# Kernel optimization log

Hardware: AMD Instinct MI355X
Metric: run time of the kernel (lower is better)

## Reference

```python
import jax, jax.numpy as jnp
import numpy as np

B, L, D = 2, 1024, 768
NH, HD = 12, 64
NL = 6
MLP = 3072
THETA = 10000.0


def _rope(pos, dim, theta):
    # pos: (L,) float -> (L, dim//2, 2, 2) rotation matrices (FLUX rope)
    omega = 1.0 / (theta ** (jnp.arange(0, dim, 2, dtype=jnp.float32) / dim))
    out = pos[:, None] * omega  # (L, dim//2)
    cos, sin = jnp.cos(out), jnp.sin(out)
    return jnp.stack([jnp.stack([cos, -sin], -1), jnp.stack([sin, cos], -1)], -2)


def _build_pe(seq_len, pe_dim):
    # 2D spatial ids: axis0 = x (fast), axis1 = y (slow); axes_dim = [pe_dim//2, pe_dim//2]
    h = w = int(seq_len ** 0.5)
    y_ids = jnp.repeat(jnp.arange(h, dtype=jnp.float32), w)
    x_ids = jnp.tile(jnp.arange(w, dtype=jnp.float32), h)
    half = pe_dim // 2
    pe = jnp.concatenate([_rope(x_ids, half, THETA), _rope(y_ids, half, THETA)], axis=-3)
    return pe[None, None]  # (1, 1, L, pe_dim//2, 2, 2)


def _apply_rope(x, pe):
    # x: (B, H, L, HD)
    xs = x.reshape(x.shape[:-1] + (-1, 1, 2))
    out = pe[..., 0] * xs[..., 0] + pe[..., 1] * xs[..., 1]
    return out.reshape(x.shape)


def _rmsnorm(x, scale):
    return x * jax.lax.rsqrt(jnp.mean(x * x, axis=-1, keepdims=True) + 1e-6) * scale


def _layernorm(x, g, b):
    m = jnp.mean(x, axis=-1, keepdims=True)
    v = jnp.var(x, axis=-1, keepdims=True)
    return (x - m) * jax.lax.rsqrt(v + 1e-5) * g + b


def _forward(spatial_features, density_weights, condition_embeddings,
             spatial_w, spatial_b, cond_w, cond_b,
             ln1_g, ln1_b, qkv_w, q_scale, k_scale, proj_w, proj_b,
             dscale, dbias, ln2_g, ln2_b, mlp_w1, mlp_b1, mlp_w2, mlp_b2,
             out_w, out_b):
    Bsz, Ls, Ds = spatial_features.shape
    x = spatial_features @ spatial_w + spatial_b
    x = x + (condition_embeddings @ cond_w + cond_b)[:, None, :]
    pe = _build_pe(Ls, HD)
    dflat = density_weights.reshape(Bsz, 1, Ls)  # H*W == L, no interpolation
    attn_scale = HD ** -0.5
    for i in range(NL):
        h = _layernorm(x, ln1_g[i], ln1_b[i])
        qkv = (h @ qkv_w[i]).reshape(Bsz, Ls, 3, NH, HD).transpose(2, 0, 3, 1, 4)
        q, k, v = qkv[0], qkv[1], qkv[2]
        q = _rmsnorm(q, q_scale[i])
        k = _rmsnorm(k, k_scale[i])
        q = _apply_rope(q, pe)
        k = _apply_rope(k, pe)
        scores = jnp.einsum('bhld,bhmd->bhlm', q, k) * attn_scale
        scores = scores + (dscale[i] * dflat[..., None] + dbias[i])  # (B,1,L,1) bcast
        attn = jax.nn.softmax(scores, axis=-1)
        o = jnp.einsum('bhlm,bhmd->bhld', attn, v)
        o = o.transpose(0, 2, 1, 3).reshape(Bsz, Ls, Ds)
        x = x + o @ proj_w[i] + proj_b[i]
        h2 = _layernorm(x, ln2_g[i], ln2_b[i])
        x = x + jax.nn.gelu(h2 @ mlp_w1[i] + mlp_b1[i], approximate=False) @ mlp_w2[i] + mlp_b2[i]
    return x @ out_w + out_b


def setup_inputs() -> dict:
    key = jax.random.key(0)
    ks = jax.random.split(key, 16)
    s = 0.02
    inp = {
        'spatial_features': jax.random.normal(ks[0], (B, L, D), jnp.float32),
        'density_weights': jax.random.uniform(ks[1], (B, 32, 32), jnp.float32),
        'condition_embeddings': jax.random.normal(ks[2], (B, 1536), jnp.float32),
        'spatial_w': jax.random.normal(ks[3], (D, D), jnp.float32) * s,
        'spatial_b': jnp.zeros((D,), jnp.float32),
        'cond_w': jax.random.normal(ks[4], (1536, D), jnp.float32) * s,
        'cond_b': jnp.zeros((D,), jnp.float32),
        'ln1_g': jnp.ones((NL, D), jnp.float32),
        'ln1_b': jnp.zeros((NL, D), jnp.float32),
        'qkv_w': jax.random.normal(ks[5], (NL, D, 3 * D), jnp.float32) * s,
        'q_scale': jnp.ones((NL, HD), jnp.float32),
        'k_scale': jnp.ones((NL, HD), jnp.float32),
        'proj_w': jax.random.normal(ks[6], (NL, D, D), jnp.float32) * s,
        'proj_b': jnp.zeros((NL, D), jnp.float32),
        'dscale': jnp.ones((NL,), jnp.float32),
        'dbias': jnp.zeros((NL,), jnp.float32),
        'ln2_g': jnp.ones((NL, D), jnp.float32),
        'ln2_b': jnp.zeros((NL, D), jnp.float32),
        'mlp_w1': jax.random.normal(ks[7], (NL, D, MLP), jnp.float32) * s,
        'mlp_b1': jnp.zeros((NL, MLP), jnp.float32),
        'mlp_w2': jax.random.normal(ks[8], (NL, MLP, D), jnp.float32) * s,
        'mlp_b2': jnp.zeros((NL, D), jnp.float32),
        'out_w': jax.random.normal(ks[9], (D, D), jnp.float32) * s,
        'out_b': jnp.zeros((D,), jnp.float32),
    }
    return inp


def reference(spatial_features, density_weights, condition_embeddings,
              spatial_w, spatial_b, cond_w, cond_b,
              ln1_g, ln1_b, qkv_w, q_scale, k_scale, proj_w, proj_b,
              dscale, dbias, ln2_g, ln2_b, mlp_w1, mlp_b1, mlp_w2, mlp_b2,
              out_w, out_b):
    return _forward(spatial_features, density_weights, condition_embeddings,
                    spatial_w, spatial_b, cond_w, cond_b,
                    ln1_g, ln1_b, qkv_w, q_scale, k_scale, proj_w, proj_b,
                    dscale, dbias, ln2_g, ln2_b, mlp_w1, mlp_b1, mlp_w2, mlp_b2,
                    out_w, out_b)
```

## Files before the change

### kernel.cpp

```cpp
#include <hip/hip_runtime.h>
#include <hip/hip_bf16.h>
#include <cstdint>
#include <cstddef>

typedef unsigned short u16;
using short8  = __attribute__((ext_vector_type(8))) short;
using floatx4 = __attribute__((ext_vector_type(4))) float;

typedef __attribute__((address_space(1))) void gvoid;
typedef __attribute__((address_space(3))) void svoid;

__device__ __forceinline__ u16 f2bf(float f) {
  __hip_bfloat16 h = __float2bfloat16(f);
  return __builtin_bit_cast(u16, h);
}

__device__ __forceinline__ floatx4 mfma16(short8 a, short8 b, floatx4 c) {
  return __builtin_amdgcn_mfma_f32_16x16x32_bf16(a, b, c, 0, 0, 0);
}

__device__ __forceinline__ void glds16(const u16* g, u16* l) {
  __builtin_amdgcn_global_load_lds((gvoid*)g, (svoid*)l, 16, 0, 0);
}

__global__ void pe_kernel(float* __restrict__ pet) {
  int t = blockIdx.x * 256 + threadIdx.x;
  if (t >= 32768) return;
  int l = t >> 5, j = t & 31;
  float pos   = (j < 16) ? (float)(l & 31) : (float)(l >> 5);
  float omega = powf(10000.f, -(float)(j & 15) / 16.f);
  float a = pos * omega;
  pet[2 * t]     = cosf(a);
  pet[2 * t + 1] = sinf(a);
}

__global__ __launch_bounds__(256) void twt_kernel(const float* __restrict__ in,
                                                  u16* __restrict__ out, int K, int N) {
  size_t lofs = (size_t)blockIdx.z * K * N;
  in  += lofs;
  out += lofs;
  __shared__ float tile[32][33];
  int bx = blockIdx.x;
  int by = blockIdx.y;
  int t = threadIdx.x;
  int lk = t >> 3, ln = (t & 7) * 4;
  float4 v = *(const float4*)(in + (size_t)(by * 32 + lk) * N + bx * 32 + ln);
  tile[lk][ln + 0] = v.x; tile[lk][ln + 1] = v.y;
  tile[lk][ln + 2] = v.z; tile[lk][ln + 3] = v.w;
  __syncthreads();
  int n = t >> 3, k0 = (t & 7) * 4;
  ushort4 o;
  o.x = f2bf(tile[k0 + 0][n]); o.y = f2bf(tile[k0 + 1][n]);
  o.z = f2bf(tile[k0 + 2][n]); o.w = f2bf(tile[k0 + 3][n]);
  *(ushort4*)(out + (size_t)(bx * 32 + n) * K + by * 32 + k0) = o;
}

__global__ void cvt_kernel(const float* __restrict__ in, u16* __restrict__ out, int n) {
  int i = blockIdx.x * 256 + threadIdx.x;
  if (i < n) out[i] = f2bf(in[i]);
}

__global__ __launch_bounds__(256) void condp_kernel(const float* __restrict__ ce,
                                                    const float* __restrict__ w,
                                                    float* __restrict__ partial) {
  int d = blockIdx.x * 256 + threadIdx.x;
  int c = blockIdx.y;
  #pragma unroll
  for (int b = 0; b < 2; b++) {
    float acc = 0.f;
    #pragma unroll 4
    for (int k = c * 96; k < c * 96 + 96; k++) acc += ce[b * 1536 + k] * w[(size_t)k * 768 + d];
    partial[(size_t)(c * 2 + b) * 768 + d] = acc;
  }
}

__global__ __launch_bounds__(256) void condr_kernel(const float* __restrict__ partial,
                                                    const float* __restrict__ bias,
                                                    float* __restrict__ out) {
  int t = blockIdx.x * 256 + threadIdx.x;
  int b = t / 768, d = t % 768;
  float acc = bias[d];
  #pragma unroll
  for (int c = 0; c < 16; c++) acc += partial[(size_t)(c * 2 + b) * 768 + d];
  out[b * 768 + d] = acc;
}

__global__ __launch_bounds__(256) void ln_kernel(const float* __restrict__ x,
                                                 const float* __restrict__ g,
                                                 const float* __restrict__ b,
                                                 u16* __restrict__ out) {
  int row = blockIdx.x;
  const float* xr = x + (size_t)row * 768;
  int t = threadIdx.x;
  float v0 = xr[t], v1 = xr[t + 256], v2 = xr[t + 512];
  float s = v0 + v1 + v2, s2 = v0 * v0 + v1 * v1 + v2 * v2;
  #pragma unroll
  for (int o = 32; o >= 1; o >>= 1) { s += __shfl_xor(s, o); s2 += __shfl_xor(s2, o); }
  __shared__ float red[8];
  int w = t >> 6, lane = t & 63;
  if (lane == 0) { red[w] = s; red[4 + w] = s2; }
  __syncthreads();
  s  = red[0] + red[1] + red[2] + red[3];
  s2 = red[4] + red[5] + red[6] + red[7];
  float mean = s * (1.f / 768.f);
  float var  = s2 * (1.f / 768.f) - mean * mean;
  float rstd = rsqrtf(var + 1e-5f);
  u16* orow = out + (size_t)row * 768;
  orow[t]       = f2bf((v0 - mean) * rstd * g[t] + b[t]);
  orow[t + 256] = f2bf((v1 - mean) * rstd * g[t + 256] + b[t + 256]);
  orow[t + 512] = f2bf((v2 - mean) * rstd * g[t + 512] + b[t + 512]);
}

__global__ __launch_bounds__(256) void vtransb_kernel(const u16* __restrict__ vb,
                                                      u16* __restrict__ vt) {
  int lt = blockIdx.x, bh = blockIdx.y;
  int b = bh / 12, h = bh % 12;
  __shared__ u16 tile[64][72];
  int t = threadIdx.x;
  int lr = t >> 2, c0 = (t & 3) * 16;
  const u16* src = vb + (size_t)(b * 1024 + lt * 64 + lr) * 768 + h * 64 + c0;
  *(short8*)&tile[lr][c0]     = *(const short8*)src;
  *(short8*)&tile[lr][c0 + 8] = *(const short8*)(src + 8);
  __syncthreads();
  int d = t >> 2, l0 = (t & 3) * 16;
  u16 o[16];
  #pragma unroll
  for (int i = 0; i < 16; i++) o[i] = tile[l0 + i][d];
  u16* dst = vt + ((size_t)bh * 64 + d) * 1024 + lt * 64 + l0;
  *(short8*)dst       = *(short8*)&o[0];
  *(short8*)(dst + 8) = *(short8*)&o[8];
}

__global__ __launch_bounds__(256) void attn_split(const u16* __restrict__ qb,
                                                  const u16* __restrict__ kbuf,
                                                  const u16* __restrict__ vt,
                                                  float* __restrict__ po,
                                                  float* __restrict__ pl) {
  const int qt = blockIdx.x, bh = blockIdx.y, sp = blockIdx.z;
  const int lane = threadIdx.x & 63, w = threadIdx.x >> 6;
  const int quad = lane >> 4, l16 = lane & 15;
  __shared__ __align__(16) u16 Ks[128 * 64];
  __shared__ __align__(16) u16 Vs[64 * 128];
  __shared__ __align__(16) u16 Ps[4][16 * 136];
  const u16* Q  = qb   + (size_t)bh * 1024 * 64;
  const u16* Kp = kbuf + (size_t)bh * 1024 * 64;
  const u16* Vp = vt   + (size_t)bh * 64 * 1024;
  const int qrow0 = qt * 64 + w * 16;
  short8 aq0, aq1;
  {
    const u16* qp = Q + (size_t)(qrow0 + l16) * 64 + quad * 8;
    aq0 = *(const short8*)qp;
    aq1 = *(const short8*)(qp + 32);
  }
  floatx4 accO[4];
  #pragma unroll
  for (int i = 0; i < 4; i++) accO[i] = (floatx4){0.f, 0.f, 0.f, 0.f};
  float lsum[4] = {0.f, 0.f, 0.f, 0.f};

  const int krow_in = (lane >> 3);
  const int kchunk  = lane & 7;
  const int vrow_in = (lane >> 4);
  const int vchunk  = lane & 15;

  for (int nt = 0; nt < 4; ++nt) {
    const int kb0 = sp * 512 + nt * 128;
    __syncthreads();
    #pragma unroll
    for (int j = 0; j < 4; j++) {
      int r = w * 32 + j * 8 + krow_in;
      int g = kchunk ^ (r & 7);
      glds16(Kp + (size_t)(kb0 + r) * 64 + g * 8, Ks + (w * 32 + j * 8) * 64);
    }
    #pragma unroll
    for (int j = 0; j < 4; j++) {
      int r = w * 16 + j * 4 + vrow_in;
      int g = vchunk ^ (r & 15);
      glds16(Vp + (size_t)r * 1024 + kb0 + g * 8, Vs + (w * 16 + j * 4) * 128);
    }
    __syncthreads();

    floatx4 s[8];
    #pragma unroll
    for (int n = 0; n < 8; n++) {
      int row = n * 16 + l16;
      int c0 = quad ^ (l16 & 7);
      short8 b0 = *(const short8*)&Ks[row * 64 + c0 * 8];
      short8 b1 = *(const short8*)&Ks[row * 64 + (c0 ^ 4) * 8];
      floatx4 z = (floatx4){0.f, 0.f, 0.f, 0.f};
      z = mfma16(aq0, b0, z);
      s[n] = mfma16(aq1, b1, z);
    }
    #pragma unroll
    for (int n = 0; n < 8; n++) {
      #pragma unroll
      for (int r = 0; r < 4; r++) {
        float pv = __expf(s[n][r] - 8.f);
        lsum[r] += pv;
        Ps[w][(quad * 4 + r) * 136 + n * 16 + l16] = f2bf(pv);
      }
    }
    #pragma unroll
    for (int kt = 0; kt < 4; kt++) {
      short8 ap = *(const short8*)&Ps[w][l16 * 136 + kt * 32 + quad * 8];
      #pragma unroll
      for (int dt = 0; dt < 4; dt++) {
        int vrow = dt * 16 + l16;
        int c = (kt * 4 + quad) ^ l16;
        short8 bv = *(const short8*)&Vs[vrow * 128 + c * 8];
        accO[dt] = mfma16(ap, bv, accO[dt]);
      }
    }
  }
  #pragma unroll
  for (int r = 0; r < 4; r++) {
    #pragma unroll
    for (int o = 1; o < 16; o <<= 1) lsum[r] += __shfl_xor(lsum[r], o);
  }
  const size_t sb = (size_t)(sp * 24 + bh) * 1024;
  #pragma unroll
  for (int r = 0; r < 4; r++) {
    int lr = qrow0 + quad * 4 + r;
    if (l16 == 0) pl[sb + lr] = lsum[r];
    #pragma unroll
    for (int dt = 0; dt < 4; dt++)
      po[(sb + lr) * 64 + dt * 16 + l16] = accO[dt][r];
  }
}

__global__ __launch_bounds__(256) void attn_comb(const float* __restrict__ po,
                                                 const float* __restrict__ pl,
                                                 u16* __restrict__ obuf) {
  int w = threadIdx.x >> 6, lane = threadIdx.x & 63;
  int gr = blockIdx.x * 4 + w;
  int bh = gr >> 10, l = gr & 1023;
  float num = 0.f, den = 0.f;
  #pragma unroll
  for (int s = 0; s < 2; s++) {
    num += po[((size_t)(s * 24 + bh) * 1024 + l) * 64 + lane];
    den += pl[(size_t)(s * 24 + bh) * 1024 + l];
  }
  int b = bh / 12, h = bh % 12;
  obuf[((size_t)(b * 1024 + l)) * 768 + h * 64 + lane] = f2bf(num / den);
}

template <int EPI, int BM, int BN>
__global__ __launch_bounds__(256) void gemm_bt(const u16* __restrict__ A,
                                               const u16* __restrict__ Bt,
                                               const float* __restrict__ bias,
                                               const float* extra,
                                               float* Cf, u16* Cb, int M, int N, int K,
                                               const float* qsc, const float* ksc,
                                               const float* petp,
                                               u16* qb, u16* kb, u16* vb) {
  constexpr int ROWS = BM + BN;
  constexpr int RPW  = ROWS / 4;
  constexpr int NG   = RPW / 8;
  constexpr int MT   = BM / 32;
  constexpr int NTW  = BN / 32;
  __shared__ __align__(16) u16 S[3][ROWS * 64];
  const int t = threadIdx.x;
  const int lane = t & 63, w = t >> 6;
  const int quad = lane >> 4, l16 = lane & 15;
  const int m0 = blockIdx.y * BM, n0 = blockIdx.x * BN;
  const int wm = (w >> 1) * (BM / 2), wn = (w & 1) * (BN / 2);

  floatx4 acc[MT][NTW];
  #pragma unroll
  for (int i = 0; i < MT; i++)
    #pragma unroll
    for (int j = 0; j < NTW; j++) acc[i][j] = (floatx4){0.f, 0.f, 0.f, 0.f};

  const u16* gsrc[NG];
  int loff[NG];
  #pragma unroll
  for (int j = 0; j < NG; j++) {
    int r = w * RPW + j * 8 + (lane >> 3);
    int c = lane & 7;
    int g = c ^ (r & 7);
    const u16* base = (r < BM) ? (A + (size_t)(m0 + r) * K)
                               : (Bt + (size_t)(n0 + r - BM) * K);
    gsrc[j] = base + g * 8;
    loff[j] = (w * RPW + j * 8) * 64;
  }

  const int NIT = K >> 6;

  auto compute = [&](int buf) {
    const u16* Sb = &S[buf][0];
    #pragma unroll
    for (int kk = 0; kk < 2; kk++) {
      short8 af[MT], bfr[NTW];
      #pragma unroll
      for (int mt = 0; mt < MT; mt++) {
        int ra = wm + mt * 16 + l16;
        af[mt] = *(const short8*)&Sb[ra * 64 + ((((kk << 2) | quad)) ^ (ra & 7)) * 8];
      }
      #pragma unroll
      for (int nt = 0; nt < NTW; nt++) {
        int rb = BM + wn + nt * 16 + l16;
        bfr[nt] = *(const short8*)&Sb[rb * 64 + ((((kk << 2) | quad)) ^ (rb & 7)) * 8];
      }
      #pragma unroll
      for (int mt = 0; mt < MT; mt++)
        #pragma unroll
        for (int nt = 0; nt < NTW; nt++)
          acc[mt][nt] = mfma16(af[mt], bfr[nt], acc[mt][nt]);
    }
  };

  #pragma unroll
  for (int j = 0; j < NG; j++) glds16(gsrc[j], &S[0][loff[j]]);
  #pragma unroll
  for (int j = 0; j < NG; j++) glds16(gsrc[j] + 64, &S[1][loff[j]]);
  asm volatile("s_waitcnt vmcnt(%0)" :: "n"(NG) : "memory");
  __builtin_amdgcn_s_barrier();
  asm volatile("" ::: "memory");

  int bufc = 0;
  for (int it = 0; it < NIT; ++it) {
    if (it + 2 < NIT) {
      int bufp = bufc + 2; if (bufp >= 3) bufp -= 3;
      #pragma unroll
      for (int j = 0; j < NG; j++) glds16(gsrc[j] + (it + 2) * 64, &S[bufp][loff[j]]);
    }
    compute(bufc);
    if (it + 1 < NIT) {
      if (it + 2 < NIT) asm volatile("s_waitcnt vmcnt(%0)" :: "n"(NG) : "memory");
      else              asm volatile("s_waitcnt vmcnt(0)" ::: "memory");
      __builtin_amdgcn_s_barrier();
      asm volatile("" ::: "memory");
    }
    bufc = (bufc + 1 == 3) ? 0 : bufc + 1;
  }

  if (EPI == 4) {
    const int cb  = n0 + wn;
    const int reg = cb / 768;
    const int hh  = (cb - reg * 768) >> 6;
    #pragma unroll
    for (int mt = 0; mt < MT; mt++) {
      #pragma unroll
      for (int r = 0; r < 4; r++) {
        int grow = m0 + wm + mt * 16 + quad * 4 + r;
        int bI = grow >> 10, lI = grow & 1023;
        if (reg < 2) {
          float s2 = 0.f;
          #pragma unroll
          for (int nt = 0; nt < NTW; nt++) s2 += acc[mt][nt][r] * acc[mt][nt][r];
          #pragma unroll
          for (int o = 1; o < 16; o <<= 1) s2 += __shfl_xor(s2, o);
          float rstd = rsqrtf(s2 * (1.f / 64.f) + 1e-6f);
          const float* sc = reg ? ksc : qsc;
          u16* dst = (reg ? kb : qb) + ((size_t)(bI * 12 + hh) * 1024 + lI) * 64;
          #pragma unroll
          for (int nt = 0; nt < NTW; nt++) {
            int d = nt * 16 + l16;
            float v = acc[mt][nt][r] * rstd * sc[d];
            float cv = petp[((lI * 32) + (d >> 1)) * 2];
            float sv = petp[((lI * 32) + (d >> 1)) * 2 + 1];
            float ov = __shfl_xor(v, 1);
            float rv = (d & 1) ? (sv * ov + cv * v) : (cv * v - sv * ov);
            if (reg == 0) rv *= 0.125f;
            dst[d] = f2bf(rv);
          }
        } else {
          u16* dst = vb + (size_t)grow * 768 + (cb - 1536);
          #pragma unroll
          for (int nt = 0; nt < NTW; nt++) dst[nt * 16 + l16] = f2bf(acc[mt][nt][r]);
        }
      }
    }
    return;
  }

  #pragma unroll
  for (int mt = 0; mt < MT; mt++) {
    #pragma unroll
    for (int nt = 0; nt < NTW; nt++) {
      int col = n0 + wn + nt * 16 + l16;
      float bcol = bias ? bias[col] : 0.f;
      #pragma unroll
      for (int r = 0; r < 4; r++) {
        int row = m0 + wm + mt * 16 + quad * 4 + r;
        float v = acc[mt][nt][r] + bcol;
        if (EPI == 1) v += extra[(row >> 10) * N + col];
        if (EPI == 2) v += extra[(size_t)row * N + col];
        if (EPI == 3) v = 0.5f * v * (1.f + erff(v * 0.70710678118654752f));
        if (Cf) Cf[(size_t)row * N + col] = v;
        if (Cb) Cb[(size_t)row * N + col] = f2bf(v);
      }
    }
  }
}

extern "C" void kernel_launch(void* const* d_in, const int* in_sizes, int n_in,
                              void* d_out, int out_size, void* d_ws, size_t ws_size,
                              hipStream_t stream) {
  const float* sf   = (const float*)d_in[0];
  const float* ce   = (const float*)d_in[2];
  const float* sw   = (const float*)d_in[3];
  const float* sb   = (const float*)d_in[4];
  const float* cw   = (const float*)d_in[5];
  const float* cb   = (const float*)d_in[6];
  const float* ln1g = (const float*)d_in[7];
  const float* ln1b = (const float*)d_in[8];
  const float* qkvw = (const float*)d_in[9];
  const float* qsc  = (const float*)d_in[10];
  const float* ksc  = (const float*)d_in[11];
  const float* pw   = (const float*)d_in[12];
  const float* pb   = (const float*)d_in[13];
  const float* ln2g = (const float*)d_in[16];
  const float* ln2b = (const float*)d_in[17];
  const float* w1   = (const float*)d_in[18];
  const float* b1   = (const float*)d_in[19];
  const float* w2   = (const float*)d_in[20];
  const float* b2   = (const float*)d_in[21];
  const float* ow   = (const float*)d_in[22];
  const float* ob   = (const float*)d_in[23];

  char* p = (char*)d_ws;
  auto alloc = [&](size_t bytes) { char* r = p; p += (bytes + 255) & ~(size_t)255; return r; };
  float* pet  = (float*)alloc((size_t)1024 * 32 * 2 * 4);
  u16* swT    = (u16*)alloc((size_t)768 * 768 * 2);
  u16* owT    = (u16*)alloc((size_t)768 * 768 * 2);
  u16* qkvT   = (u16*)alloc((size_t)6 * 2304 * 768 * 2);
  u16* pwT    = (u16*)alloc((size_t)6 * 768 * 768 * 2);
  u16* w1T    = (u16*)alloc((size_t)6 * 3072 * 768 * 2);
  u16* w2T    = (u16*)alloc((size_t)6 * 768 * 3072 * 2);
  u16* sfb    = (u16*)alloc((size_t)2048 * 768 * 2);
  float* cpar = (float*)alloc((size_t)32 * 768 * 4);
  float* cond = (float*)alloc((size_t)2 * 768 * 4);
  float* x    = (float*)alloc((size_t)2048 * 768 * 4);
  u16* xb     = (u16*)alloc((size_t)2048 * 768 * 2);
  u16* h      = (u16*)alloc((size_t)2048 * 768 * 2);
  u16* qbuf   = (u16*)alloc((size_t)2048 * 768 * 2);
  u16* kbuf   = (u16*)alloc((size_t)2048 * 768 * 2);
  u16* vb     = (u16*)alloc((size_t)2048 * 768 * 2);
  u16* vtb    = (u16*)alloc((size_t)2048 * 768 * 2);
  u16* obuf   = (u16*)alloc((size_t)2048 * 768 * 2);
  u16* gbuf   = (u16*)alloc((size_t)2048 * 3072 * 2);
  float* po   = (float*)alloc((size_t)2 * 24 * 1024 * 64 * 4);
  float* pl   = (float*)alloc((size_t)2 * 24 * 1024 * 4);

  pe_kernel<<<128, 256, 0, stream>>>(pet);
  twt_kernel<<<dim3(24, 24, 1), 256, 0, stream>>>(sw, swT, 768, 768);
  twt_kernel<<<dim3(24, 24, 1), 256, 0, stream>>>(ow, owT, 768, 768);
  twt_kernel<<<dim3(72, 24, 6), 256, 0, stream>>>(qkvw, qkvT, 768, 2304);
  twt_kernel<<<dim3(24, 24, 6), 256, 0, stream>>>(pw, pwT, 768, 768);
  twt_kernel<<<dim3(96, 24, 6), 256, 0, stream>>>(w1, w1T, 768, 3072);
  twt_kernel<<<dim3(24, 96, 6), 256, 0, stream>>>(w2, w2T, 3072, 768);
  cvt_kernel<<<(2048 * 768) / 256, 256, 0, stream>>>(sf, sfb, 2048 * 768);
  condp_kernel<<<dim3(3, 16), 256, 0, stream>>>(ce, cw, cpar);
  condr_kernel<<<6, 256, 0, stream>>>(cpar, cb, cond);

  gemm_bt<1, 64, 64><<<dim3(12, 32), 256, 0, stream>>>(sfb, swT, sb, cond, x, nullptr,
      2048, 768, 768, nullptr, nullptr, nullptr, nullptr, nullptr, nullptr);

  for (int i = 0; i < 6; i++) {
    ln_kernel<<<2048, 256, 0, stream>>>(x, ln1g + i * 768, ln1b + i * 768, h);
    gemm_bt<4, 64, 128><<<dim3(18, 32), 256, 0, stream>>>(h, qkvT + (size_t)i * 2304 * 768,
        nullptr, nullptr, nullptr, nullptr, 2048, 2304, 768,
        qsc + i * 64, ksc + i * 64, pet, qbuf, kbuf, vb);
    vtransb_kernel<<<dim3(16, 24), 256, 0, stream>>>(vb, vtb);
    attn_split<<<dim3(16, 24, 2), 256, 0, stream>>>(qbuf, kbuf, vtb, po, pl);
    attn_comb<<<6144, 256, 0, stream>>>(po, pl, obuf);
    gemm_bt<2, 64, 64><<<dim3(12, 32), 256, 0, stream>>>(obuf, pwT + (size_t)i * 768 * 768,
        pb + i * 768, x, x, xb, 2048, 768, 768,
        nullptr, nullptr, nullptr, nullptr, nullptr, nullptr);
    ln_kernel<<<2048, 256, 0, stream>>>(x, ln2g + i * 768, ln2b + i * 768, h);
    gemm_bt<3, 64, 128><<<dim3(24, 32), 256, 0, stream>>>(h, w1T + (size_t)i * 3072 * 768,
        b1 + i * 3072, nullptr, nullptr, gbuf, 2048, 3072, 768,
        nullptr, nullptr, nullptr, nullptr, nullptr, nullptr);
    gemm_bt<2, 64, 64><<<dim3(12, 32), 256, 0, stream>>>(gbuf, w2T + (size_t)i * 768 * 3072,
        b2 + i * 768, x, x, xb, 2048, 768, 3072,
        nullptr, nullptr, nullptr, nullptr, nullptr, nullptr);
  }
  gemm_bt<0, 64, 64><<<dim3(12, 32), 256, 0, stream>>>(xb, owT, ob, nullptr, (float*)d_out, nullptr,
      2048, 768, 768, nullptr, nullptr, nullptr, nullptr, nullptr, nullptr);
}
```

Measured before the change: 994.4 us.

## Fuse V transpose into QKV epilogue and attention combine into projection GEMM

The QKV GEMM epilogue now writes V directly in transposed per-head layout through shared memory, which removes the separate transpose kernel and the vb buffer. The projection GEMM loads its A operand by summing the two attention split partials and dividing by the summed denominators on the fly. This drops the attn_comb kernel and the obuf round trip. Two warps do the A staging through registers while the other two issue async loads for B, and this path uses double buffering instead of triple. The bf16 copy of x is now written only on the last layer, where the output GEMM needs it. The trade-off is extra load and convert work inside the GEMM prologue, with less pipelining depth.

```diff
diff --git a/kernel.cpp b/kernel.cpp
--- a/kernel.cpp
+++ b/kernel.cpp
@@ -109,26 +109,6 @@
   orow[t]       = f2bf((v0 - mean) * rstd * g[t] + b[t]);
   orow[t + 256] = f2bf((v1 - mean) * rstd * g[t + 256] + b[t + 256]);
   orow[t + 512] = f2bf((v2 - mean) * rstd * g[t + 512] + b[t + 512]);
-}
-
-__global__ __launch_bounds__(256) void vtransb_kernel(const u16* __restrict__ vb,
-                                                      u16* __restrict__ vt) {
-  int lt = blockIdx.x, bh = blockIdx.y;
-  int b = bh / 12, h = bh % 12;
-  __shared__ u16 tile[64][72];
-  int t = threadIdx.x;
-  int lr = t >> 2, c0 = (t & 3) * 16;
-  const u16* src = vb + (size_t)(b * 1024 + lt * 64 + lr) * 768 + h * 64 + c0;
-  *(short8*)&tile[lr][c0]     = *(const short8*)src;
-  *(short8*)&tile[lr][c0 + 8] = *(const short8*)(src + 8);
-  __syncthreads();
-  int d = t >> 2, l0 = (t & 3) * 16;
-  u16 o[16];
-  #pragma unroll
-  for (int i = 0; i < 16; i++) o[i] = tile[l0 + i][d];
-  u16* dst = vt + ((size_t)bh * 64 + d) * 1024 + lt * 64 + l0;
-  *(short8*)dst       = *(short8*)&o[0];
-  *(short8*)(dst + 8) = *(short8*)&o[8];
 }
 
 __global__ __launch_bounds__(256) void attn_split(const u16* __restrict__ qb,
@@ -227,23 +207,7 @@
   }
 }
 
-__global__ __launch_bounds__(256) void attn_comb(const float* __restrict__ po,
-                                                 const float* __restrict__ pl,
-                                                 u16* __restrict__ obuf) {
-  int w = threadIdx.x >> 6, lane = threadIdx.x & 63;
-  int gr = blockIdx.x * 4 + w;
-  int bh = gr >> 10, l = gr & 1023;
-  float num = 0.f, den = 0.f;
-  #pragma unroll
-  for (int s = 0; s < 2; s++) {
-    num += po[((size_t)(s * 24 + bh) * 1024 + l) * 64 + lane];
-    den += pl[(size_t)(s * 24 + bh) * 1024 + l];
-  }
-  int b = bh / 12, h = bh % 12;
-  obuf[((size_t)(b * 1024 + l)) * 768 + h * 64 + lane] = f2bf(num / den);
-}
-
-template <int EPI, int BM, int BN>
+template <int EPI, int BM, int BN, bool AFUSE>
 __global__ __launch_bounds__(256) void gemm_bt(const u16* __restrict__ A,
                                                const u16* __restrict__ Bt,
                                                const float* __restrict__ bias,
@@ -251,13 +215,15 @@
                                                float* Cf, u16* Cb, int M, int N, int K,
                                                const float* qsc, const float* ksc,
                                                const float* petp,
-                                               u16* qb, u16* kb, u16* vb) {
+                                               u16* qb, u16* kb, u16* vt,
+                                               const float* po, const float* pl) {
   constexpr int ROWS = BM + BN;
   constexpr int RPW  = ROWS / 4;
   constexpr int NG   = RPW / 8;
   constexpr int MT   = BM / 32;
   constexpr int NTW  = BN / 32;
-  __shared__ __align__(16) u16 S[3][ROWS * 64];
+  constexpr int NBUF = AFUSE ? 2 : 3;
+  __shared__ __align__(16) u16 S[NBUF][ROWS * 64];
   const int t = threadIdx.x;
   const int lane = t & 63, w = t >> 6;
   const int quad = lane >> 4, l16 = lane & 15;
@@ -308,34 +274,124 @@
     }
   };
 
-  #pragma unroll
-  for (int j = 0; j < NG; j++) glds16(gsrc[j], &S[0][loff[j]]);
-  #pragma unroll
-  for (int j = 0; j < NG; j++) glds16(gsrc[j] + 64, &S[1][loff[j]]);
-  asm volatile("s_waitcnt vmcnt(%0)" :: "n"(NG) : "memory");
-  __builtin_amdgcn_s_barrier();
-  asm volatile("" ::: "memory");
-
-  int bufc = 0;
-  for (int it = 0; it < NIT; ++it) {
-    if (it + 2 < NIT) {
-      int bufp = bufc + 2; if (bufp >= 3) bufp -= 3;
-      #pragma unroll
-      for (int j = 0; j < NG; j++) glds16(gsrc[j] + (it + 2) * 64, &S[bufp][loff[j]]);
-    }
-    compute(bufc);
-    if (it + 1 < NIT) {
-      if (it + 2 < NIT) asm volatile("s_waitcnt vmcnt(%0)" :: "n"(NG) : "memory");
-      else              asm volatile("s_waitcnt vmcnt(0)" ::: "memory");
-      __builtin_amdgcn_s_barrier();
-      asm volatile("" ::: "memory");
-    }
-    bufc = (bufc + 1 == 3) ? 0 : bufc + 1;
+  if constexpr (AFUSE) {
+    __shared__ float den[768];
+    const int blk = m0 >> 10, l0 = m0 & 1023;
+    for (int q = t; q < 768; q += 256) {
+      int hh = q >> 6, r = q & 63;
+      float d0 = pl[((size_t)(blk * 12 + hh)) * 1024 + l0 + r];
+      float d1 = pl[((size_t)(24 + blk * 12 + hh)) * 1024 + l0 + r];
+      den[q] = 1.f / (d0 + d1);
+    }
+    __syncthreads();
+
+    const int ar = w * 32 + (lane >> 3);
+    const int ac = lane & 7;
+    float4 regs[16];
+
+    auto stageA = [&](int it) {
+      #pragma unroll
+      for (int j = 0; j < 4; j++) {
+        int r = ar + j * 8;
+        size_t base = ((size_t)(blk * 12 + it) * 1024 + l0 + r) * 64 + ac * 8;
+        regs[j * 4 + 0] = *(const float4*)(po + base);
+        regs[j * 4 + 1] = *(const float4*)(po + base + 4);
+        regs[j * 4 + 2] = *(const float4*)(po + base + (size_t)24 * 65536);
+        regs[j * 4 + 3] = *(const float4*)(po + base + 4 + (size_t)24 * 65536);
+      }
+    };
+    auto writeA = [&](int it, int buf) {
+      #pragma unroll
+      for (int j = 0; j < 4; j++) {
+        int r = ar + j * 8;
+        float dv = den[it * 64 + r];
+        u16 o[8];
+        float4 a0 = regs[j * 4 + 0], a1 = regs[j * 4 + 1];
+        float4 b0 = regs[j * 4 + 2], b1 = regs[j * 4 + 3];
+        o[0] = f2bf((a0.x + b0.x) * dv); o[1] = f2bf((a0.y + b0.y) * dv);
+        o[2] = f2bf((a0.z + b0.z) * dv); o[3] = f2bf((a0.w + b0.w) * dv);
+        o[4] = f2bf((a1.x + b1.x) * dv); o[5] = f2bf((a1.y + b1.y) * dv);
+        o[6] = f2bf((a1.z + b1.z) * dv); o[7] = f2bf((a1.w + b1.w) * dv);
+        *(short8*)&S[buf][r * 64 + (ac ^ (r & 7)) * 8] = *(short8*)o;
+      }
+    };
+
+    if (w < 2) { stageA(0); writeA(0, 0); }
+    else {
+      #pragma unroll
+      for (int j = 0; j < NG; j++) glds16(gsrc[j], &S[0][loff[j]]);
+    }
+    __syncthreads();
+
+    int cur = 0;
+    for (int it = 0; it < 12; ++it) {
+      if (it + 1 < 12) {
+        if (w < 2) stageA(it + 1);
+        else {
+          #pragma unroll
+          for (int j = 0; j < NG; j++) glds16(gsrc[j] + (it + 1) * 64, &S[cur ^ 1][loff[j]]);
+        }
+      }
+      compute(cur);
+      if (it + 1 < 12) {
+        if (w < 2) writeA(it + 1, cur ^ 1);
+        __syncthreads();
+      }
+      cur ^= 1;
+    }
+  } else {
+    #pragma unroll
+    for (int j = 0; j < NG; j++) glds16(gsrc[j], &S[0][loff[j]]);
+    #pragma unroll
+    for (int j = 0; j < NG; j++) glds16(gsrc[j] + 64, &S[1][loff[j]]);
+    asm volatile("s_waitcnt vmcnt(%0)" :: "n"(NG) : "memory");
+    __builtin_amdgcn_s_barrier();
+    asm volatile("" ::: "memory");
+
+    int bufc = 0;
+    for (int it = 0; it < NIT; ++it) {
+      if (it + 2 < NIT) {
+        int bufp = bufc + 2; if (bufp >= 3) bufp -= 3;
+        #pragma unroll
+        for (int j = 0; j < NG; j++) glds16(gsrc[j] + (it + 2) * 64, &S[bufp][loff[j]]);
+      }
+      compute(bufc);
+      if (it + 1 < NIT) {
+        if (it + 2 < NIT) asm volatile("s_waitcnt vmcnt(%0)" :: "n"(NG) : "memory");
+        else              asm volatile("s_waitcnt vmcnt(0)" ::: "memory");
+        __builtin_amdgcn_s_barrier();
+        asm volatile("" ::: "memory");
+      }
+      bufc = (bufc + 1 == 3) ? 0 : bufc + 1;
+    }
   }
 
   if (EPI == 4) {
+    const int reg = n0 / 768;
+    if (reg == 2) {
+      __syncthreads();
+      u16* T = (u16*)&S[0][0];
+      #pragma unroll
+      for (int mt = 0; mt < MT; mt++)
+        #pragma unroll
+        for (int nt = 0; nt < NTW; nt++)
+          #pragma unroll
+          for (int r = 0; r < 4; r++)
+            T[(wm + mt * 16 + quad * 4 + r) * 130 + wn + nt * 16 + l16] =
+                f2bf(acc[mt][nt][r]);
+      __syncthreads();
+      int d = t >> 1, lh = (t & 1) * 32;
+      int head = ((n0 - 1536) >> 6) + (d >> 6), d63 = d & 63;
+      u16 o[32];
+      #pragma unroll
+      for (int i2 = 0; i2 < 32; i2++) o[i2] = T[(lh + i2) * 130 + d];
+      u16* dst = vt + ((size_t)((m0 >> 10) * 12 + head) * 64 + d63) * 1024
+                    + (m0 & 1023) + lh;
+      #pragma unroll
+      for (int i2 = 0; i2 < 4; i2++) *(short8*)(dst + i2 * 8) = *(short8*)&o[i2 * 8];
+      return;
+    }
     const int cb  = n0 + wn;
-    const int reg = cb / 768;
     const int hh  = (cb - reg * 768) >> 6;
     #pragma unroll
     for (int mt = 0; mt < MT; mt++) {
@@ -343,30 +399,24 @@
       for (int r = 0; r < 4; r++) {
         int grow = m0 + wm + mt * 16 + quad * 4 + r;
         int bI = grow >> 10, lI = grow & 1023;
-        if (reg < 2) {
-          float s2 = 0.f;
-          #pragma unroll
-          for (int nt = 0; nt < NTW; nt++) s2 += acc[mt][nt][r] * acc[mt][nt][r];
-          #pragma unroll
-          for (int o = 1; o < 16; o <<= 1) s2 += __shfl_xor(s2, o);
-          float rstd = rsqrtf(s2 * (1.f / 64.f) + 1e-6f);
-          const float* sc = reg ? ksc : qsc;
-          u16* dst = (reg ? kb : qb) + ((size_t)(bI * 12 + hh) * 1024 + lI) * 64;
-          #pragma unroll
-          for (int nt = 0; nt < NTW; nt++) {
-            int d = nt * 16 + l16;
-            float v = acc[mt][nt][r] * rstd * sc[d];
-            float cv = petp[((lI * 32) + (d >> 1)) * 2];
-            float sv = petp[((lI * 32) + (d >> 1)) * 2 + 1];
-            float ov = __shfl_xor(v, 1);
-            float rv = (d & 1) ? (sv * ov + cv * v) : (cv * v - sv * ov);
-            if (reg == 0) rv *= 0.125f;
-            dst[d] = f2bf(rv);
-          }
-        } else {
-          u16* dst = vb + (size_t)grow * 768 + (cb - 1536);
-          #pragma unroll
-          for (int nt = 0; nt < NTW; nt++) dst[nt * 16 + l16] = f2bf(acc[mt][nt][r]);
+        float s2 = 0.f;
+        #pragma unroll
+        for (int nt = 0; nt < NTW; nt++) s2 += acc[mt][nt][r] * acc[mt][nt][r];
+        #pragma unroll
+        for (int o = 1; o < 16; o <<= 1) s2 += __shfl_xor(s2, o);
+        float rstd = rsqrtf(s2 * (1.f / 64.f) + 1e-6f);
+        const float* sc = reg ? ksc : qsc;
+        u16* dst = (reg ? kb : qb) + ((size_t)(bI * 12 + hh) * 1024 + lI) * 64;
+        #pragma unroll
+        for (int nt = 0; nt < NTW; nt++) {
+          int d = nt * 16 + l16;
+          float v = acc[mt][nt][r] * rstd * sc[d];
+          float cv = petp[((lI * 32) + (d >> 1)) * 2];
+          float sv = petp[((lI * 32) + (d >> 1)) * 2 + 1];
+          float ov = __shfl_xor(v, 1);
+          float rv = (d & 1) ? (sv * ov + cv * v) : (cv * v - sv * ov);
+          if (reg == 0) rv *= 0.125f;
+          dst[d] = f2bf(rv);
         }
       }
     }
@@ -435,9 +485,7 @@
   u16* h      = (u16*)alloc((size_t)2048 * 768 * 2);
   u16* qbuf   = (u16*)alloc((size_t)2048 * 768 * 2);
   u16* kbuf   = (u16*)alloc((size_t)2048 * 768 * 2);
-  u16* vb     = (u16*)alloc((size_t)2048 * 768 * 2);
   u16* vtb    = (u16*)alloc((size_t)2048 * 768 * 2);
-  u16* obuf   = (u16*)alloc((size_t)2048 * 768 * 2);
   u16* gbuf   = (u16*)alloc((size_t)2048 * 3072 * 2);
   float* po   = (float*)alloc((size_t)2 * 24 * 1024 * 64 * 4);
   float* pl   = (float*)alloc((size_t)2 * 24 * 1024 * 4);
@@ -453,28 +501,26 @@
   condp_kernel<<<dim3(3, 16), 256, 0, stream>>>(ce, cw, cpar);
   condr_kernel<<<6, 256, 0, stream>>>(cpar, cb, cond);
 
-  gemm_bt<1, 64, 64><<<dim3(12, 32), 256, 0, stream>>>(sfb, swT, sb, cond, x, nullptr,
-      2048, 768, 768, nullptr, nullptr, nullptr, nullptr, nullptr, nullptr);
+  gemm_bt<1, 64, 64, false><<<dim3(12, 32), 256, 0, stream>>>(sfb, swT, sb, cond, x, nullptr,
+      2048, 768, 768, nullptr, nullptr, nullptr, nullptr, nullptr, nullptr, nullptr, nullptr);
 
   for (int i = 0; i < 6; i++) {
     ln_kernel<<<2048, 256, 0, stream>>>(x, ln1g + i * 768, ln1b + i * 768, h);
-    gemm_bt<4, 64, 128><<<dim3(18, 32), 256, 0, stream>>>(h, qkvT + (size_t)i * 2304 * 768,
+    gemm_bt<4, 64, 128, false><<<dim3(18, 32), 256, 0, stream>>>(h, qkvT + (size_t)i * 2304 * 768,
         nullptr, nullptr, nullptr, nullptr, 2048, 2304, 768,
-        qsc + i * 64, ksc + i * 64, pet, qbuf, kbuf, vb);
-    vtransb_kernel<<<dim3(16, 24), 256, 0, stream>>>(vb, vtb);
+        qsc + i * 64, ksc + i * 64, pet, qbuf, kbuf, vtb, nullptr, nullptr);
     attn_split<<<dim3(16, 24, 2), 256, 0, stream>>>(qbuf, kbuf, vtb, po, pl);
-    attn_comb<<<6144, 256, 0, stream>>>(po, pl, obuf);
-    gemm_bt<2, 64, 64><<<dim3(12, 32), 256, 0, stream>>>(obuf, pwT + (size_t)i * 768 * 768,
-        pb + i * 768, x, x, xb, 2048, 768, 768,
-        nullptr, nullptr, nullptr, nullptr, nullptr, nullptr);
+    gemm_bt<2, 64, 64, true><<<dim3(12, 32), 256, 0, stream>>>(h, pwT + (size_t)i * 768 * 768,
+        pb + i * 768, x, x, nullptr, 2048, 768, 768,
+        nullptr, nullptr, nullptr, nullptr, nullptr, nullptr, po, pl);
     ln_kernel<<<2048, 256, 0, stream>>>(x, ln2g + i * 768, ln2b + i * 768, h);
-    gemm_bt<3, 64, 128><<<dim3(24, 32), 256, 0, stream>>>(h, w1T + (size_t)i * 3072 * 768,
+    gemm_bt<3, 64, 128, false><<<dim3(24, 32), 256, 0, stream>>>(h, w1T + (size_t)i * 3072 * 768,
         b1 + i * 3072, nullptr, nullptr, gbuf, 2048, 3072, 768,
-        nullptr, nullptr, nullptr, nullptr, nullptr, nullptr);
-    gemm_bt<2, 64, 64><<<dim3(12, 32), 256, 0, stream>>>(gbuf, w2T + (size_t)i * 768 * 3072,
-        b2 + i * 768, x, x, xb, 2048, 768, 3072,
-        nullptr, nullptr, nullptr, nullptr, nullptr, nullptr);
-  }
-  gemm_bt<0, 64, 64><<<dim3(12, 32), 256, 0, stream>>>(xb, owT, ob, nullptr, (float*)d_out, nullptr,
-      2048, 768, 768, nullptr, nullptr, nullptr, nullptr, nullptr, nullptr);
-}
+        nullptr, nullptr, nullptr, nullptr, nullptr, nullptr, nullptr, nullptr);
+    gemm_bt<2, 64, 64, false><<<dim3(12, 32), 256, 0, stream>>>(gbuf, w2T + (size_t)i * 768 * 3072,
+        b2 + i * 768, x, x, (i == 5) ? xb : nullptr, 2048, 768, 3072,
+        nullptr, nullptr, nullptr, nullptr, nullptr, nullptr, nullptr, nullptr);
+  }
+  gemm_bt<0, 64, 64, false><<<dim3(12, 32), 256, 0, stream>>>(xb, owT, ob, nullptr, (float*)d_out, nullptr,
+      2048, 768, 768, nullptr, nullptr, nullptr, nullptr, nullptr, nullptr, nullptr, nullptr);
+}
```

After: 1.005 ms. Within noise of the previous version (+1.1%).

## Fuse V transpose into QKV GEMM epilogue and drop attention split-combine

Applied to the files above, without the earlier changes.

The QKV GEMM epilogue now writes V directly in transposed layout through shared memory, which removes the separate transpose kernel and its intermediate buffer. Attention becomes a single-pass kernel: 128 threads per block, 32 query rows per block, looping over all 1024 keys and normalizing in place. This replaces the split-K partial outputs and the combine kernel. The bf16 copy of x is now written only after the last layer. The trade is fewer launches and less fp32 intermediate traffic against longer per-block serial KV loops and smaller blocks.

```diff
diff --git a/kernel.cpp b/kernel.cpp
--- a/kernel.cpp
+++ b/kernel.cpp
@@ -111,41 +111,20 @@
   orow[t + 512] = f2bf((v2 - mean) * rstd * g[t + 512] + b[t + 512]);
 }
 
-__global__ __launch_bounds__(256) void vtransb_kernel(const u16* __restrict__ vb,
-                                                      u16* __restrict__ vt) {
-  int lt = blockIdx.x, bh = blockIdx.y;
-  int b = bh / 12, h = bh % 12;
-  __shared__ u16 tile[64][72];
-  int t = threadIdx.x;
-  int lr = t >> 2, c0 = (t & 3) * 16;
-  const u16* src = vb + (size_t)(b * 1024 + lt * 64 + lr) * 768 + h * 64 + c0;
-  *(short8*)&tile[lr][c0]     = *(const short8*)src;
-  *(short8*)&tile[lr][c0 + 8] = *(const short8*)(src + 8);
-  __syncthreads();
-  int d = t >> 2, l0 = (t & 3) * 16;
-  u16 o[16];
-  #pragma unroll
-  for (int i = 0; i < 16; i++) o[i] = tile[l0 + i][d];
-  u16* dst = vt + ((size_t)bh * 64 + d) * 1024 + lt * 64 + l0;
-  *(short8*)dst       = *(short8*)&o[0];
-  *(short8*)(dst + 8) = *(short8*)&o[8];
-}
-
-__global__ __launch_bounds__(256) void attn_split(const u16* __restrict__ qb,
-                                                  const u16* __restrict__ kbuf,
-                                                  const u16* __restrict__ vt,
-                                                  float* __restrict__ po,
-                                                  float* __restrict__ pl) {
-  const int qt = blockIdx.x, bh = blockIdx.y, sp = blockIdx.z;
+__global__ __launch_bounds__(128) void attn_one(const u16* __restrict__ qb,
+                                                const u16* __restrict__ kbuf,
+                                                const u16* __restrict__ vt,
+                                                u16* __restrict__ obuf) {
+  const int qt = blockIdx.x, bh = blockIdx.y;
   const int lane = threadIdx.x & 63, w = threadIdx.x >> 6;
   const int quad = lane >> 4, l16 = lane & 15;
   __shared__ __align__(16) u16 Ks[128 * 64];
   __shared__ __align__(16) u16 Vs[64 * 128];
-  __shared__ __align__(16) u16 Ps[4][16 * 136];
+  __shared__ __align__(16) u16 Ps[2][16 * 136];
   const u16* Q  = qb   + (size_t)bh * 1024 * 64;
   const u16* Kp = kbuf + (size_t)bh * 1024 * 64;
   const u16* Vp = vt   + (size_t)bh * 64 * 1024;
-  const int qrow0 = qt * 64 + w * 16;
+  const int qrow0 = qt * 32 + w * 16;
   short8 aq0, aq1;
   {
     const u16* qp = Q + (size_t)(qrow0 + l16) * 64 + quad * 8;
@@ -162,20 +141,20 @@
   const int vrow_in = (lane >> 4);
   const int vchunk  = lane & 15;
 
-  for (int nt = 0; nt < 4; ++nt) {
-    const int kb0 = sp * 512 + nt * 128;
+  for (int nt = 0; nt < 8; ++nt) {
+    const int kb0 = nt * 128;
     __syncthreads();
     #pragma unroll
-    for (int j = 0; j < 4; j++) {
-      int r = w * 32 + j * 8 + krow_in;
+    for (int j = 0; j < 8; j++) {
+      int r = w * 64 + j * 8 + krow_in;
       int g = kchunk ^ (r & 7);
-      glds16(Kp + (size_t)(kb0 + r) * 64 + g * 8, Ks + (w * 32 + j * 8) * 64);
-    }
-    #pragma unroll
-    for (int j = 0; j < 4; j++) {
-      int r = w * 16 + j * 4 + vrow_in;
+      glds16(Kp + (size_t)(kb0 + r) * 64 + g * 8, Ks + (w * 64 + j * 8) * 64);
+    }
+    #pragma unroll
+    for (int j = 0; j < 8; j++) {
+      int r = w * 32 + j * 4 + vrow_in;
       int g = vchunk ^ (r & 15);
-      glds16(Vp + (size_t)r * 1024 + kb0 + g * 8, Vs + (w * 16 + j * 4) * 128);
+      glds16(Vp + (size_t)r * 1024 + kb0 + g * 8, Vs + (w * 32 + j * 4) * 128);
     }
     __syncthreads();
 
@@ -216,31 +195,15 @@
     #pragma unroll
     for (int o = 1; o < 16; o <<= 1) lsum[r] += __shfl_xor(lsum[r], o);
   }
-  const size_t sb = (size_t)(sp * 24 + bh) * 1024;
+  const int b = bh / 12, h = bh % 12;
   #pragma unroll
   for (int r = 0; r < 4; r++) {
     int lr = qrow0 + quad * 4 + r;
-    if (l16 == 0) pl[sb + lr] = lsum[r];
-    #pragma unroll
-    for (int dt = 0; dt < 4; dt++)
-      po[(sb + lr) * 64 + dt * 16 + l16] = accO[dt][r];
-  }
-}
-
-__global__ __launch_bounds__(256) void attn_comb(const float* __restrict__ po,
-                                                 const float* __restrict__ pl,
-                                                 u16* __restrict__ obuf) {
-  int w = threadIdx.x >> 6, lane = threadIdx.x & 63;
-  int gr = blockIdx.x * 4 + w;
-  int bh = gr >> 10, l = gr & 1023;
-  float num = 0.f, den = 0.f;
-  #pragma unroll
-  for (int s = 0; s < 2; s++) {
-    num += po[((size_t)(s * 24 + bh) * 1024 + l) * 64 + lane];
-    den += pl[(size_t)(s * 24 + bh) * 1024 + l];
-  }
-  int b = bh / 12, h = bh % 12;
-  obuf[((size_t)(b * 1024 + l)) * 768 + h * 64 + lane] = f2bf(num / den);
+    float inv = 1.f / lsum[r];
+    u16* dst = obuf + ((size_t)(b * 1024 + lr)) * 768 + h * 64;
+    #pragma unroll
+    for (int dt = 0; dt < 4; dt++) dst[dt * 16 + l16] = f2bf(accO[dt][r] * inv);
+  }
 }
 
 template <int EPI, int BM, int BN>
@@ -251,7 +214,7 @@
                                                float* Cf, u16* Cb, int M, int N, int K,
                                                const float* qsc, const float* ksc,
                                                const float* petp,
-                                               u16* qb, u16* kb, u16* vb) {
+                                               u16* qb, u16* kb, u16* vt) {
   constexpr int ROWS = BM + BN;
   constexpr int RPW  = ROWS / 4;
   constexpr int NG   = RPW / 8;
@@ -334,39 +297,56 @@
   }
 
   if (EPI == 4) {
-    const int cb  = n0 + wn;
-    const int reg = cb / 768;
-    const int hh  = (cb - reg * 768) >> 6;
+    const int reg = n0 / 768;
+    if (reg == 2) {
+      __syncthreads();
+      u16* T = (u16*)&S[0][0];
+      #pragma unroll
+      for (int mt = 0; mt < MT; mt++)
+        #pragma unroll
+        for (int nt = 0; nt < NTW; nt++)
+          #pragma unroll
+          for (int r = 0; r < 4; r++)
+            T[(wm + mt * 16 + quad * 4 + r) * 130 + wn + nt * 16 + l16] =
+                f2bf(acc[mt][nt][r]);
+      __syncthreads();
+      int d = t >> 1, lh = (t & 1) * 32;
+      int head = ((n0 - 1536) >> 6) + (d >> 6), d63 = d & 63;
+      u16 o[32];
+      #pragma unroll
+      for (int i2 = 0; i2 < 32; i2++) o[i2] = T[(lh + i2) * 130 + d];
+      u16* dst = vt + ((size_t)((m0 >> 10) * 12 + head) * 64 + d63) * 1024
+                    + (m0 & 1023) + lh;
+      #pragma unroll
+      for (int i2 = 0; i2 < 4; i2++) *(short8*)(dst + i2 * 8) = *(short8*)&o[i2 * 8];
+      return;
+    }
+    const int cbase = n0 + wn;
+    const int hh  = (cbase - reg * 768) >> 6;
     #pragma unroll
     for (int mt = 0; mt < MT; mt++) {
       #pragma unroll
       for (int r = 0; r < 4; r++) {
         int grow = m0 + wm + mt * 16 + quad * 4 + r;
         int bI = grow >> 10, lI = grow & 1023;
-        if (reg < 2) {
-          float s2 = 0.f;
-          #pragma unroll
-          for (int nt = 0; nt < NTW; nt++) s2 += acc[mt][nt][r] * acc[mt][nt][r];
-          #pragma unroll
-          for (int o = 1; o < 16; o <<= 1) s2 += __shfl_xor(s2, o);
-          float rstd = rsqrtf(s2 * (1.f / 64.f) + 1e-6f);
-          const float* sc = reg ? ksc : qsc;
-          u16* dst = (reg ? kb : qb) + ((size_t)(bI * 12 + hh) * 1024 + lI) * 64;
-          #pragma unroll
-          for (int nt = 0; nt < NTW; nt++) {
-            int d = nt * 16 + l16;
-            float v = acc[mt][nt][r] * rstd * sc[d];
-            float cv = petp[((lI * 32) + (d >> 1)) * 2];
-            float sv = petp[((lI * 32) + (d >> 1)) * 2 + 1];
-            float ov = __shfl_xor(v, 1);
-            float rv = (d & 1) ? (sv * ov + cv * v) : (cv * v - sv * ov);
-            if (reg == 0) rv *= 0.125f;
-            dst[d] = f2bf(rv);
-          }
-        } else {
-          u16* dst = vb + (size_t)grow * 768 + (cb - 1536);
-          #pragma unroll
-          for (int nt = 0; nt < NTW; nt++) dst[nt * 16 + l16] = f2bf(acc[mt][nt][r]);
+        float s2 = 0.f;
+        #pragma unroll
+        for (int nt = 0; nt < NTW; nt++) s2 += acc[mt][nt][r] * acc[mt][nt][r];
+        #pragma unroll
+        for (int o = 1; o < 16; o <<= 1) s2 += __shfl_xor(s2, o);
+        float rstd = rsqrtf(s2 * (1.f / 64.f) + 1e-6f);
+        const float* sc = reg ? ksc : qsc;
+        u16* dst = (reg ? kb : qb) + ((size_t)(bI * 12 + hh) * 1024 + lI) * 64;
+        #pragma unroll
+        for (int nt = 0; nt < NTW; nt++) {
+          int d = nt * 16 + l16;
+          float v = acc[mt][nt][r] * rstd * sc[d];
+          float cv = petp[((lI * 32) + (d >> 1)) * 2];
+          float sv = petp[((lI * 32) + (d >> 1)) * 2 + 1];
+          float ov = __shfl_xor(v, 1);
+          float rv = (d & 1) ? (sv * ov + cv * v) : (cv * v - sv * ov);
+          if (reg == 0) rv *= 0.125f;
+          dst[d] = f2bf(rv);
         }
       }
     }
@@ -435,12 +415,9 @@
   u16* h      = (u16*)alloc((size_t)2048 * 768 * 2);
   u16* qbuf   = (u16*)alloc((size_t)2048 * 768 * 2);
   u16* kbuf   = (u16*)alloc((size_t)2048 * 768 * 2);
-  u16* vb     = (u16*)alloc((size_t)2048 * 768 * 2);
   u16* vtb    = (u16*)alloc((size_t)2048 * 768 * 2);
   u16* obuf   = (u16*)alloc((size_t)2048 * 768 * 2);
   u16* gbuf   = (u16*)alloc((size_t)2048 * 3072 * 2);
-  float* po   = (float*)alloc((size_t)2 * 24 * 1024 * 64 * 4);
-  float* pl   = (float*)alloc((size_t)2 * 24 * 1024 * 4);
 
   pe_kernel<<<128, 256, 0, stream>>>(pet);
   twt_kernel<<<dim3(24, 24, 1), 256, 0, stream>>>(sw, swT, 768, 768);
@@ -460,19 +437,17 @@
     ln_kernel<<<2048, 256, 0, stream>>>(x, ln1g + i * 768, ln1b + i * 768, h);
     gemm_bt<4, 64, 128><<<dim3(18, 32), 256, 0, stream>>>(h, qkvT + (size_t)i * 2304 * 768,
         nullptr, nullptr, nullptr, nullptr, 2048, 2304, 768,
-        qsc + i * 64, ksc + i * 64, pet, qbuf, kbuf, vb);
-    vtransb_kernel<<<dim3(16, 24), 256, 0, stream>>>(vb, vtb);
-    attn_split<<<dim3(16, 24, 2), 256, 0, stream>>>(qbuf, kbuf, vtb, po, pl);
-    attn_comb<<<6144, 256, 0, stream>>>(po, pl, obuf);
+        qsc + i * 64, ksc + i * 64, pet, qbuf, kbuf, vtb);
+    attn_one<<<dim3(32, 24), 128, 0, stream>>>(qbuf, kbuf, vtb, obuf);
     gemm_bt<2, 64, 64><<<dim3(12, 32), 256, 0, stream>>>(obuf, pwT + (size_t)i * 768 * 768,
-        pb + i * 768, x, x, xb, 2048, 768, 768,
+        pb + i * 768, x, x, nullptr, 2048, 768, 768,
         nullptr, nullptr, nullptr, nullptr, nullptr, nullptr);
     ln_kernel<<<2048, 256, 0, stream>>>(x, ln2g + i * 768, ln2b + i * 768, h);
     gemm_bt<3, 64, 128><<<dim3(24, 32), 256, 0, stream>>>(h, w1T + (size_t)i * 3072 * 768,
         b1 + i * 3072, nullptr, nullptr, gbuf, 2048, 3072, 768,
         nullptr, nullptr, nullptr, nullptr, nullptr, nullptr);
     gemm_bt<2, 64, 64><<<dim3(12, 32), 256, 0, stream>>>(gbuf, w2T + (size_t)i * 768 * 3072,
-        b2 + i * 768, x, x, xb, 2048, 768, 3072,
+        b2 + i * 768, x, x, (i == 5) ? xb : nullptr, 2048, 768, 3072,
         nullptr, nullptr, nullptr, nullptr, nullptr, nullptr);
   }
   gemm_bt<0, 64, 64><<<dim3(12, 32), 256, 0, stream>>>(xb, owT, ob, nullptr, (float*)d_out, nullptr,
```

Result: faster. 967.3 us (-2.7%).
